# Kernel tuning notes

Measured on AMD Instinct MI355X. Metric: run time of the kernel, lower is better.

The kernel has to match this reference:

```python
import jax, jax.numpy as jnp
import numpy as np

N = 100000   # nodes per type
E = 500000   # edges per edge type
HID = 128    # hidden_channels
H = 4        # heads
D = HID // H # head dim = 32
L = 2        # layers
T = 2        # node types: 0=user, 1=item
R = 2        # edge types: 0=user->item, 1=item->user


def setup_inputs() -> dict:
    key = jax.random.key(0)
    ks = jax.random.split(key, 16)
    s = jnp.float32(0.05)
    f32 = jnp.float32
    return {
        "x_user": jax.random.normal(ks[0], (N, HID), f32),
        "x_item": jax.random.normal(ks[1], (N, HID), f32),
        "W_in": jax.random.normal(ks[2], (T, HID, HID), f32) * s,
        "b_in": jnp.zeros((T, HID), f32),
        "Wk": jax.random.normal(ks[3], (L, T, HID, HID), f32) * s,
        "bk": jnp.zeros((L, T, HID), f32),
        "Wq": jax.random.normal(ks[4], (L, T, HID, HID), f32) * s,
        "bq": jnp.zeros((L, T, HID), f32),
        "Wv": jax.random.normal(ks[5], (L, T, HID, HID), f32) * s,
        "bv": jnp.zeros((L, T, HID), f32),
        "a_rel": jax.random.normal(ks[6], (L, R, H, D, D), f32) * s,
        "m_rel": jax.random.normal(ks[7], (L, R, H, D, D), f32) * s,
        "p_rel": jnp.ones((L, R, H), f32),
        "Wo": jax.random.normal(ks[8], (L, T, HID, HID), f32) * s,
        "bo": jnp.zeros((L, T, HID), f32),
        "skip": jnp.zeros((L, T), f32),
        "edge_ui": jax.random.randint(ks[9], (2, E), 0, N, dtype=jnp.int32),
        "edge_iu": jax.random.randint(ks[10], (2, E), 0, N, dtype=jnp.int32),
    }


def _seg_softmax(logits, seg, n):
    # numerically stable softmax over edges grouped by destination node
    m = jax.ops.segment_max(logits, seg, num_segments=n)            # [N,H]
    m = jnp.where(jnp.isfinite(m), m, jnp.float32(0.0))
    e = jnp.exp(logits - m[seg])                                    # [E,H]
    z = jax.ops.segment_sum(e, seg, num_segments=n)                 # [N,H]
    return e / (z[seg] + jnp.float32(1e-16))


def reference(x_user, x_item, W_in, b_in, Wk, bk, Wq, bq, Wv, bv,
              a_rel, m_rel, p_rel, Wo, bo, skip, edge_ui, edge_iu):
    scale = jnp.float32(1.0 / np.sqrt(D))
    # per-node-type input linear + relu (lin_dict)
    h = [jax.nn.relu(x_user @ W_in[0] + b_in[0]),
         jax.nn.relu(x_item @ W_in[1] + b_in[1])]
    # (edge_type_id, src_type, dst_type, edge_index)
    etypes = [(0, 0, 1, edge_ui), (1, 1, 0, edge_iu)]
    for l in range(L):
        k = [(h[t] @ Wk[l, t] + bk[l, t]).reshape(N, H, D) for t in range(T)]
        q = [(h[t] @ Wq[l, t] + bq[l, t]).reshape(N, H, D) for t in range(T)]
        v = [(h[t] @ Wv[l, t] + bv[l, t]).reshape(N, H, D) for t in range(T)]
        agg = [jnp.zeros((N, H, D), h[0].dtype) for _ in range(T)]
        for r, st, dt, e in etypes:
            src, dst = e[0], e[1]
            # relation-specific transforms applied on node table (N < E)
            k_r = jnp.einsum('nhd,hde->nhe', k[st], a_rel[l, r])
            v_r = jnp.einsum('nhd,hde->nhe', v[st], m_rel[l, r])
            logits = jnp.sum(q[dt][dst] * k_r[src], axis=-1) * p_rel[l, r] * scale  # [E,H]
            alpha = _seg_softmax(logits, dst, N)                                    # [E,H]
            msg = alpha[:, :, None] * v_r[src]                                      # [E,H,D]
            agg[dt] = agg[dt] + jax.ops.segment_sum(msg, dst, num_segments=N)
        h_new = []
        for t in range(T):
            out = agg[t].reshape(N, HID)
            a = jax.nn.gelu(out, approximate=False) @ Wo[l, t] + bo[l, t]
            beta = jax.nn.sigmoid(skip[l, t])
            hn = beta * a + (1.0 - beta) * h[t]
            if l > 0:  # model-level residual (i > 0 in torch code)
                hn = hn + h[t]
            h_new.append(hn)
        h = h_new
    return jnp.stack(h)  # [T, N, HID]
```

## Files before the change

kernel.cpp:

```cpp
#include <hip/hip_runtime.h>
#include <stdint.h>
#include <stdio.h>

#define NN 100000
#define NE 500000
#define HID 128
#define NH 4
#define HD 32
#define LL 2
#define SCANB 1024
#define NB ((NN + SCANB - 1) / SCANB)

typedef unsigned short u16;
typedef unsigned char u8;
typedef unsigned int u32;
typedef __attribute__((ext_vector_type(8))) short bfrag;
typedef __attribute__((ext_vector_type(4))) float f32x4;
typedef __attribute__((ext_vector_type(2))) float f32x2;

__device__ __forceinline__ float b2f(u32 lo16) {
  union { u32 u; float f; } c; c.u = lo16; return c.f;
}
__device__ __forceinline__ u16 f2b(float f) {
  union { float f; u32 u; } c; c.f = f;
  u32 u = c.u;
  u32 r = (u + 0x7FFFu + ((u >> 16) & 1u)) >> 16;
  return (u16)r;
}
__device__ __forceinline__ float geluf(float x) {
  return 0.5f * x * (1.0f + erff(x * 0.70710678118654752f));
}
__device__ __forceinline__ void up8(uint4 a, float* f) {
  f[0] = b2f(a.x << 16); f[1] = b2f(a.x & 0xFFFF0000u);
  f[2] = b2f(a.y << 16); f[3] = b2f(a.y & 0xFFFF0000u);
  f[4] = b2f(a.z << 16); f[5] = b2f(a.z & 0xFFFF0000u);
  f[6] = b2f(a.w << 16); f[7] = b2f(a.w & 0xFFFF0000u);
}

__global__ __launch_bounds__(256) void csr_count(const int* __restrict__ e0,
                                                 const int* __restrict__ e1,
                                                 int* __restrict__ deg) {
  int r = blockIdx.y;
  const int* edges = r ? e1 : e0;
  int e = blockIdx.x * 256 + threadIdx.x;
  if (e < NE) atomicAdd(&deg[(size_t)r * NN + edges[NE + e]], 1);
}

__global__ __launch_bounds__(SCANB) void scan1(const int* __restrict__ deg,
                                               int* __restrict__ rp,
                                               int* __restrict__ bsum) {
  __shared__ int ls[SCANB];
  int r = blockIdx.y;
  int t = threadIdx.x;
  int g = blockIdx.x * SCANB + t;
  int v = (g < NN) ? deg[(size_t)r * NN + g] : 0;
  ls[t] = v;
  __syncthreads();
#pragma unroll
  for (int off = 1; off < SCANB; off <<= 1) {
    int u = (t >= off) ? ls[t - off] : 0;
    __syncthreads();
    ls[t] += u;
    __syncthreads();
  }
  if (g < NN) rp[(size_t)r * (NN + 1) + g] = ls[t] - v;
  if (t == SCANB - 1) bsum[r * NB + blockIdx.x] = ls[t];
}

__global__ __launch_bounds__(128) void scan2(const int* __restrict__ bsum,
                                             int* __restrict__ boff) {
  __shared__ int ls[128];
  int r = blockIdx.y;
  int t = threadIdx.x;
  int v = (t < NB) ? bsum[r * NB + t] : 0;
  ls[t] = v;
  __syncthreads();
#pragma unroll
  for (int off = 1; off < 128; off <<= 1) {
    int u = (t >= off) ? ls[t - off] : 0;
    __syncthreads();
    ls[t] += u;
    __syncthreads();
  }
  if (t < NB) boff[r * NB + t] = ls[t] - v;
}

__global__ __launch_bounds__(SCANB) void scan3(int* __restrict__ rp,
                                               int* __restrict__ cursor,
                                               const int* __restrict__ boff) {
  int r = blockIdx.y;
  int g = blockIdx.x * SCANB + threadIdx.x;
  if (g < NN) {
    int v = rp[(size_t)r * (NN + 1) + g] + boff[r * NB + blockIdx.x];
    rp[(size_t)r * (NN + 1) + g] = v;
    cursor[(size_t)r * NN + g] = v;
  }
  if (g == 0) rp[(size_t)r * (NN + 1) + NN] = NE;
}

__global__ __launch_bounds__(256) void csr_fill(const int* __restrict__ e0,
                                                const int* __restrict__ e1,
                                                int* __restrict__ cursor,
                                                int* __restrict__ s0,
                                                int* __restrict__ s1) {
  int r = blockIdx.y;
  const int* edges = r ? e1 : e0;
  int* srcs = r ? s1 : s0;
  int e = blockIdx.x * 256 + threadIdx.x;
  if (e < NE) {
    int pos = atomicAdd(&cursor[(size_t)r * NN + edges[NE + e]], 1);
    srcs[pos] = edges[e];
  }
}

__global__ __launch_bounds__(256) void hist_deg(const int* __restrict__ rp,
                                                int* __restrict__ hist) {
  __shared__ int lh[64];
  int r = blockIdx.y;
  if (threadIdx.x < 64) lh[threadIdx.x] = 0;
  __syncthreads();
  int d = blockIdx.x * 256 + threadIdx.x;
  if (d < NN) {
    const int* rowptr = rp + (size_t)r * (NN + 1);
    int dg = rowptr[d + 1] - rowptr[d];
    atomicAdd(&lh[dg < 63 ? dg : 63], 1);
  }
  __syncthreads();
  if (threadIdx.x < 64 && lh[threadIdx.x])
    atomicAdd(&hist[r * 64 + threadIdx.x], lh[threadIdx.x]);
}

__global__ __launch_bounds__(64) void scan_hist(const int* __restrict__ hist,
                                                int* __restrict__ hcur) {
  __shared__ int ls[64];
  int r = blockIdx.y;
  int t = threadIdx.x;
  int v = hist[r * 64 + t];
  ls[t] = v;
  __syncthreads();
#pragma unroll
  for (int off = 1; off < 64; off <<= 1) {
    int u = (t >= off) ? ls[t - off] : 0;
    __syncthreads();
    ls[t] += u;
    __syncthreads();
  }
  hcur[r * 64 + t] = ls[t] - v;
}

__global__ __launch_bounds__(256) void scatter_deg(const int* __restrict__ rp,
                                                   int* __restrict__ hcur,
                                                   int* __restrict__ o0,
                                                   int* __restrict__ o1) {
  __shared__ int lh[64];
  __shared__ int lbase[64];
  int r = blockIdx.y;
  int* order = r ? o1 : o0;
  if (threadIdx.x < 64) lh[threadIdx.x] = 0;
  __syncthreads();
  int d = blockIdx.x * 256 + threadIdx.x;
  int dg = 0, rank = 0;
  if (d < NN) {
    const int* rowptr = rp + (size_t)r * (NN + 1);
    dg = rowptr[d + 1] - rowptr[d];
    if (dg > 63) dg = 63;
    rank = atomicAdd(&lh[dg], 1);
  }
  __syncthreads();
  if (threadIdx.x < 64)
    lbase[threadIdx.x] = lh[threadIdx.x] ? atomicAdd(&hcur[r * 64 + threadIdx.x], lh[threadIdx.x]) : 0;
  __syncthreads();
  if (d < NN) order[lbase[dg] + rank] = d;
}

__global__ __launch_bounds__(256) void prep_wT(const float* __restrict__ src, size_t srcStride,
                                               u16* __restrict__ dst, size_t dstStride,
                                               const float* __restrict__ bsrc, int bsStride,
                                               float* __restrict__ bdst, int bdStride,
                                               const float* __restrict__ p_rel_q) {
  int m = blockIdx.y;
  const float* S = src + (size_t)m * srcStride;
  u16* D = dst + (size_t)m * dstStride;
  int idx = blockIdx.x * 256 + threadIdx.x;
  int k = idx >> 7, n = idx & 127;
  float v = S[idx];
  if (p_rel_q != nullptr) {
    int l = m >> 1, t = m & 1;
    v *= p_rel_q[((l << 1) | (1 - t)) * NH + (n >> 5)] * 0.17677669529663687f;
  }
  D[(size_t)n * HID + k] = f2b(v);
  if (bsrc != nullptr && blockIdx.x == 0 && threadIdx.x < HID) {
    int col = threadIdx.x;
    float bvv = bsrc[(size_t)m * bsStride + col];
    if (p_rel_q != nullptr) {
      int l = m >> 1, t = m & 1;
      bvv *= p_rel_q[((l << 1) | (1 - t)) * NH + (col >> 5)] * 0.17677669529663687f;
    }
    bdst[(size_t)m * bdStride + col] = bvv;
  }
}

__global__ __launch_bounds__(256) void combine_all(
    const float* __restrict__ Wk, const float* __restrict__ bk,
    const float* __restrict__ Wv, const float* __restrict__ bv,
    const float* __restrict__ a_rel, const float* __restrict__ m_rel,
    u16* __restrict__ wqkvT, float* __restrict__ bqkv) {
  int l = blockIdx.z;
  int t = blockIdx.y >> 1, which = blockIdx.y & 1;
  const float* W  = (which == 0 ? Wk : Wv) + (size_t)(l * 2 + t) * HID * HID;
  const float* b  = (which == 0 ? bk : bv) + (size_t)(l * 2 + t) * HID;
  const float* Ar = (which == 0 ? a_rel : m_rel) + (size_t)(l * 2 + t) * NH * HD * HD;
  u16* Wd = wqkvT + ((size_t)(l * 2 + t) * 3 + 1 + which) * HID * HID;
  float* bd = bqkv + ((size_t)(l * 2 + t) * 3 + 1 + which) * HID;
  int idx = blockIdx.x * 256 + threadIdx.x;
  int i = idx >> 7, col = idx & 127;
  int h = col >> 5, e = col & 31;
  {
    const float* ap = Ar + h * HD * HD + e;
    const float* wp = W + (size_t)i * HID + h * HD;
    float s = 0.f;
#pragma unroll
    for (int d = 0; d < HD; ++d) s += wp[d] * ap[d * HD];
    Wd[(size_t)col * HID + i] = f2b(s);
  }
  if (blockIdx.x == 0 && threadIdx.x < HID) {
    int col2 = threadIdx.x, h2 = col2 >> 5, e2 = col2 & 31;
    const float* ap = Ar + h2 * HD * HD + e2;
    const float* bp = b + h2 * HD;
    float s = 0.f;
#pragma unroll
    for (int d = 0; d < HD; ++d) s += bp[d] * ap[d * HD];
    bd[col2] = s;
  }
}

__global__ __launch_bounds__(256) void qkv_gemm(
    const u16* __restrict__ h0, const u16* __restrict__ h1,
    const u16* __restrict__ WT,
    const float* __restrict__ bias,
    u16* __restrict__ q0, u16* __restrict__ q1,
    u8* __restrict__ k0, u8* __restrict__ k1,
    u8* __restrict__ v0, u8* __restrict__ v1, int gb) {
  __shared__ __align__(16) u16 sW[2][HID * HID];
  const int t = blockIdx.x >= gb;
  const int bx = t ? blockIdx.x - gb : blockIdx.x;
  const u16* A = t ? h1 : h0;
  const u16* Wg = WT + (size_t)t * 3 * HID * HID;
  const float* bs = bias + (size_t)t * 3 * HID;
  u16* Oq = t ? q1 : q0;
  u8* Ok = t ? k1 : k0;
  u8* Ov = t ? v1 : v0;

  const int lane = threadIdx.x & 63;
  const int wid = threadIdx.x >> 6;
  const int l16 = lane & 15, g = lane >> 4;
  const int rbase = bx * 128 + wid * 32;

  auto stageW = [&](int m, int buf) {
    const u16* Wm = Wg + (size_t)m * HID * HID;
#pragma unroll
    for (int j = 0; j < 8; ++j) {
      int ins = wid * 8 + j;
      int o16 = ins * 64 + lane;
      int row = o16 >> 4, ch = o16 & 15;
      const u16* src = Wm + (size_t)row * HID + ((ch ^ (row & 7)) << 3);
      u16* dst = &sW[buf][0] + (size_t)ins * 512;
      __builtin_amdgcn_global_load_lds(
          (const __attribute__((address_space(1))) unsigned int*)src,
          (__attribute__((address_space(3))) unsigned int*)dst, 16, 0, 0);
    }
  };

  bfrag af[2][4];
  int rowA[2];
#pragma unroll
  for (int rt = 0; rt < 2; ++rt) {
    int row = rbase + rt * 16 + l16;
    rowA[rt] = row;
    int rl = row < NN ? row : NN - 1;
    const bfrag* ap = (const bfrag*)(A + (size_t)rl * HID);
#pragma unroll
    for (int ks = 0; ks < 4; ++ks) af[rt][ks] = ap[ks * 4 + g];
  }

  stageW(0, 0);
  __syncthreads();

#pragma unroll
  for (int m = 0; m < 3; ++m) {
    if (m + 1 < 3) stageW(m + 1, (m + 1) & 1);
    f32x4 acc[2][8];
#pragma unroll
    for (int rt = 0; rt < 2; ++rt)
#pragma unroll
      for (int ct = 0; ct < 8; ++ct) acc[rt][ct] = (f32x4){0.f, 0.f, 0.f, 0.f};
#pragma unroll
    for (int ct = 0; ct < 8; ++ct) {
      int row = ct * 16 + l16;
      bfrag wf[4];
#pragma unroll
      for (int ks = 0; ks < 4; ++ks)
        wf[ks] = *(const bfrag*)&sW[m & 1][(size_t)row * HID +
                                           (((ks * 4 + g) ^ (row & 7)) << 3)];
#pragma unroll
      for (int ks = 0; ks < 4; ++ks)
#pragma unroll
        for (int rt = 0; rt < 2; ++rt)
          acc[rt][ct] = __builtin_amdgcn_mfma_f32_16x16x32_bf16(wf[ks], af[rt][ks],
                                                                acc[rt][ct], 0, 0, 0);
    }
#pragma unroll
    for (int rt = 0; rt < 2; ++rt) {
      int row = rowA[rt];
      if (row >= NN) continue;
#pragma unroll
      for (int ct = 0; ct < 8; ++ct) {
        int nc = ct * 16 + g * 4;
        const float4 bb = *(const float4*)(bs + m * HID + nc);
        float o0 = acc[rt][ct][0] + bb.x;
        float o1 = acc[rt][ct][1] + bb.y;
        float o2 = acc[rt][ct][2] + bb.z;
        float o3 = acc[rt][ct][3] + bb.w;
        if (m == 0) {
          u32 lo = (u32)f2b(o0) | ((u32)f2b(o1) << 16);
          u32 hi = (u32)f2b(o2) | ((u32)f2b(o3) << 16);
          *(uint2*)(Oq + (size_t)row * HID + nc) = make_uint2(lo, hi);
        } else {
          u8* O8 = (m == 1) ? Ok : Ov;
          u32 pk = __builtin_amdgcn_cvt_pk_fp8_f32(o0, o1, 0u, false);
          pk = __builtin_amdgcn_cvt_pk_fp8_f32(o2, o3, pk, true);
          *(u32*)(O8 + (size_t)row * HID + nc) = pk;
        }
      }
    }
    if (m + 1 < 3) __syncthreads();
  }
}

template <int NMAT, bool RELU, bool SKIP, bool FP8KV, bool AF32>
__global__ __launch_bounds__(256) void mfgemm(
    const void* __restrict__ A0, const void* __restrict__ A1, int M, int gb,
    const u16* __restrict__ WT, size_t wtStride,
    const float* __restrict__ bias, size_t biasStride,
    u16* __restrict__ O00, u16* __restrict__ O01, u16* __restrict__ O02,
    u16* __restrict__ O10, u16* __restrict__ O11, u16* __restrict__ O12,
    float* __restrict__ Of0, float* __restrict__ Of1,
    const u16* __restrict__ hp0, const u16* __restrict__ hp1,
    const float* __restrict__ skipP, int resflag) {
  __shared__ __align__(16) u16 sW[HID * HID];
  const int t = blockIdx.x >= gb;
  const int bx = t ? blockIdx.x - gb : blockIdx.x;
  const void* A = t ? A1 : A0;
  const u16* Wg = WT + (size_t)t * wtStride;
  const float* bs = bias + (size_t)t * biasStride;
  u16* Os[3];
  Os[0] = t ? O10 : O00; Os[1] = t ? O11 : O01; Os[2] = t ? O12 : O02;
  float* Of = t ? Of1 : Of0;
  const u16* hprev = t ? hp1 : hp0;

  const int lane = threadIdx.x & 63;
  const int wid = threadIdx.x >> 6;
  const int l16 = lane & 15, g = lane >> 4;
  const int rbase = bx * 128 + wid * 32;

  float beta = 0.f;
  if (SKIP) beta = 1.f / (1.f + __expf(-skipP[t]));

  auto stageW = [&](int m) {
    const u16* Wm = Wg + (size_t)m * HID * HID;
#pragma unroll
    for (int j = 0; j < 8; ++j) {
      int ins = wid * 8 + j;
      int o16 = ins * 64 + lane;
      int row = o16 >> 4, ch = o16 & 15;
      const u16* src = Wm + (size_t)row * HID + ((ch ^ (row & 7)) << 3);
      u16* dst = sW + (size_t)ins * 512;
      __builtin_amdgcn_global_load_lds(
          (const __attribute__((address_space(1))) unsigned int*)src,
          (__attribute__((address_space(3))) unsigned int*)dst, 16, 0, 0);
    }
  };

  bfrag af[2][4];
  int rowA[2];
#pragma unroll
  for (int rt = 0; rt < 2; ++rt) {
    int row = rbase + rt * 16 + l16;
    rowA[rt] = row;
    int rl = row < M ? row : M - 1;
    if (AF32) {
      const float* apf = (const float*)A + (size_t)rl * HID;
#pragma unroll
      for (int ks = 0; ks < 4; ++ks) {
        float4 u0 = *(const float4*)(apf + (ks * 4 + g) * 8);
        float4 u1 = *(const float4*)(apf + (ks * 4 + g) * 8 + 4);
        union { u16 s[8]; bfrag b; } pk;
        pk.s[0] = f2b(u0.x); pk.s[1] = f2b(u0.y); pk.s[2] = f2b(u0.z); pk.s[3] = f2b(u0.w);
        pk.s[4] = f2b(u1.x); pk.s[5] = f2b(u1.y); pk.s[6] = f2b(u1.z); pk.s[7] = f2b(u1.w);
        af[rt][ks] = pk.b;
      }
    } else {
      const bfrag* ap = (const bfrag*)A + (size_t)rl * (HID / 8);
#pragma unroll
      for (int ks = 0; ks < 4; ++ks) af[rt][ks] = ap[ks * 4 + g];
    }
  }

  stageW(0);
  __syncthreads();

#pragma unroll
  for (int m = 0; m < NMAT; ++m) {
    f32x4 acc[2][8];
#pragma unroll
    for (int rt = 0; rt < 2; ++rt)
#pragma unroll
      for (int ct = 0; ct < 8; ++ct) acc[rt][ct] = (f32x4){0.f, 0.f, 0.f, 0.f};
#pragma unroll
    for (int ct = 0; ct < 8; ++ct) {
      int row = ct * 16 + l16;
      bfrag wf[4];
#pragma unroll
      for (int ks = 0; ks < 4; ++ks)
        wf[ks] = *(const bfrag*)&sW[(size_t)row * HID + (((ks * 4 + g) ^ (row & 7)) << 3)];
#pragma unroll
      for (int ks = 0; ks < 4; ++ks)
#pragma unroll
        for (int rt = 0; rt < 2; ++rt)
          acc[rt][ct] = __builtin_amdgcn_mfma_f32_16x16x32_bf16(wf[ks], af[rt][ks],
                                                                acc[rt][ct], 0, 0, 0);
    }
    if (m + 1 < NMAT) {
      __syncthreads();
      stageW(m + 1);
    }
    u16* Ob = Os[m];
#pragma unroll
    for (int rt = 0; rt < 2; ++rt) {
      int row = rowA[rt];
      if (row >= M) continue;
#pragma unroll
      for (int ct = 0; ct < 8; ++ct) {
        int nc = ct * 16 + g * 4;
        const float4 bb = *(const float4*)(bs + m * HID + nc);
        float o0 = acc[rt][ct][0] + bb.x;
        float o1 = acc[rt][ct][1] + bb.y;
        float o2 = acc[rt][ct][2] + bb.z;
        float o3 = acc[rt][ct][3] + bb.w;
        if (RELU) {
          o0 = fmaxf(o0, 0.f); o1 = fmaxf(o1, 0.f);
          o2 = fmaxf(o2, 0.f); o3 = fmaxf(o3, 0.f);
        }
        if (SKIP) {
          uint2 hh2 = *(const uint2*)(hprev + (size_t)row * HID + nc);
          float h0 = b2f(hh2.x << 16), h1 = b2f(hh2.x & 0xFFFF0000u);
          float h2 = b2f(hh2.y << 16), h3 = b2f(hh2.y & 0xFFFF0000u);
          o0 = beta * o0 + (1.f - beta) * h0;
          o1 = beta * o1 + (1.f - beta) * h1;
          o2 = beta * o2 + (1.f - beta) * h2;
          o3 = beta * o3 + (1.f - beta) * h3;
          if (resflag) { o0 += h0; o1 += h1; o2 += h2; o3 += h3; }
        }
        if (FP8KV && m >= 1) {
          u32 pk = __builtin_amdgcn_cvt_pk_fp8_f32(o0, o1, 0u, false);
          pk = __builtin_amdgcn_cvt_pk_fp8_f32(o2, o3, pk, true);
          *(u32*)((u8*)Ob + (size_t)row * HID + nc) = pk;
        } else {
          if (Ob != nullptr) {
            u32 lo = (u32)f2b(o0) | ((u32)f2b(o1) << 16);
            u32 hi = (u32)f2b(o2) | ((u32)f2b(o3) << 16);
            *(uint2*)(Ob + (size_t)row * HID + nc) = make_uint2(lo, hi);
          }
          if (NMAT == 1 && Of != nullptr) {
            *(float4*)(Of + (size_t)row * HID + nc) = make_float4(o0, o1, o2, o3);
          }
        }
      }
    }
    if (m + 1 < NMAT) __syncthreads();
  }
}

__global__ __launch_bounds__(256) void agg_csr(
    const int* __restrict__ rp0, const int* __restrict__ ss0, const int* __restrict__ od0,
    const u16* __restrict__ q0, const u8* __restrict__ k0,
    const u8* __restrict__ v0, u16* __restrict__ o0,
    const int* __restrict__ rp1, const int* __restrict__ ss1, const int* __restrict__ od1,
    const u16* __restrict__ q1, const u8* __restrict__ k1,
    const u8* __restrict__ v1, u16* __restrict__ o1, int agb) {
  const int r = blockIdx.x >= agb;
  const int bx = r ? blockIdx.x - agb : blockIdx.x;
  int i = bx * 256 + threadIdx.x;
  if (i >= NN * NH) return;
  const int* rowptr = r ? rp1 : rp0;
  const int* srcs = r ? ss1 : ss0;
  const int* order = r ? od1 : od0;
  const u16* qT = r ? q1 : q0;
  const u8* kT = r ? k1 : k0;
  const u8* vT = r ? v1 : v0;
  u16* aggb = r ? o1 : o0;

  int dst = order[i >> 2], h = i & 3;
  float qv[HD];
  {
    const uint4* qp = (const uint4*)(qT + (size_t)dst * HID + h * HD);
#pragma unroll
    for (int j = 0; j < 4; ++j) up8(qp[j], qv + j * 8);
  }
  float acc[HD];
#pragma unroll
  for (int j = 0; j < HD; ++j) acc[j] = 0.f;
  float z = 0.f;
  int b = rowptr[dst], e2 = rowptr[dst + 1];
  for (int idx = b; idx < e2; ++idx) {
    int src = srcs[idx];
    const uint4* kp = (const uint4*)(kT + (size_t)src * HID + h * HD);
    const uint4* vp = (const uint4*)(vT + (size_t)src * HID + h * HD);
    uint4 ka0 = kp[0], ka1 = kp[1];
    uint4 va0 = vp[0], va1 = vp[1];
    u32 kw[8] = {ka0.x, ka0.y, ka0.z, ka0.w, ka1.x, ka1.y, ka1.z, ka1.w};
    u32 vw[8] = {va0.x, va0.y, va0.z, va0.w, va1.x, va1.y, va1.z, va1.w};
    float s = 0.f;
#pragma unroll
    for (int j = 0; j < 8; ++j) {
      f32x2 p0 = __builtin_amdgcn_cvt_pk_f32_fp8(kw[j], false);
      f32x2 p1 = __builtin_amdgcn_cvt_pk_f32_fp8(kw[j], true);
      s += qv[4 * j] * p0.x + qv[4 * j + 1] * p0.y + qv[4 * j + 2] * p1.x + qv[4 * j + 3] * p1.y;
    }
    s = fminf(s, 60.f);
    float ev = __expf(s);
    z += ev;
#pragma unroll
    for (int j = 0; j < 8; ++j) {
      f32x2 p0 = __builtin_amdgcn_cvt_pk_f32_fp8(vw[j], false);
      f32x2 p1 = __builtin_amdgcn_cvt_pk_f32_fp8(vw[j], true);
      acc[4 * j] += ev * p0.x; acc[4 * j + 1] += ev * p0.y;
      acc[4 * j + 2] += ev * p1.x; acc[4 * j + 3] += ev * p1.y;
    }
  }
  float inv = 1.f / (z + 1e-16f);
  u16* ap = aggb + (size_t)dst * HID + h * HD;
  u32 w[16];
#pragma unroll
  for (int j = 0; j < 16; ++j) {
    float a0 = geluf(acc[2 * j] * inv);
    float a1 = geluf(acc[2 * j + 1] * inv);
    w[j] = (u32)f2b(a0) | ((u32)f2b(a1) << 16);
  }
#pragma unroll
  for (int j = 0; j < 4; ++j)
    *(uint4*)(ap + j * 8) = make_uint4(w[4 * j], w[4 * j + 1], w[4 * j + 2], w[4 * j + 3]);
}

extern "C" void kernel_launch(void* const* d_in, const int* in_sizes, int n_in,
                              void* d_out, int out_size, void* d_ws, size_t ws_size,
                              hipStream_t stream) {
  const float* x_user = (const float*)d_in[0];
  const float* x_item = (const float*)d_in[1];
  const float* W_in = (const float*)d_in[2];
  const float* b_in = (const float*)d_in[3];
  const float* Wk = (const float*)d_in[4];
  const float* bk = (const float*)d_in[5];
  const float* Wq = (const float*)d_in[6];
  const float* bq = (const float*)d_in[7];
  const float* Wv = (const float*)d_in[8];
  const float* bv = (const float*)d_in[9];
  const float* a_rel = (const float*)d_in[10];
  const float* m_rel = (const float*)d_in[11];
  const float* p_rel = (const float*)d_in[12];
  const float* Wo = (const float*)d_in[13];
  const float* bo = (const float*)d_in[14];
  const float* skipP = (const float*)d_in[15];
  const int* edge_ui = (const int*)d_in[16];
  const int* edge_iu = (const int*)d_in[17];
  float* out = (float*)d_out;

  char* p = (char*)d_ws;
  auto take = [&](size_t bytes) {
    void* r = (void*)p;
    p += (bytes + 255) & ~(size_t)255;
    return r;
  };
  size_t nodeB = (size_t)NN * HID * sizeof(u16);
  size_t node8 = (size_t)NN * HID;
  u16* hb[2] = {(u16*)take(nodeB), (u16*)take(nodeB)};
  u16* qb[2] = {(u16*)take(nodeB), (u16*)take(nodeB)};
  u8* kb[2] = {(u8*)take(node8), (u8*)take(node8)};
  u8* vb[2] = {(u8*)take(node8), (u8*)take(node8)};
  u16* aggb[2] = {(u16*)take(nodeB), (u16*)take(nodeB)};
  int* deg2   = (int*)take((size_t)2 * NN * 4);
  int* cur2   = (int*)take((size_t)2 * NN * 4);
  int* bsum2  = (int*)take((size_t)2 * NB * 4);
  int* boff2  = (int*)take((size_t)2 * NB * 4);
  int* hist2  = (int*)take((size_t)2 * 64 * 4);
  int* hcur2  = (int*)take((size_t)2 * 64 * 4);
  int* rp2    = (int*)take((size_t)2 * (NN + 1) * 4);
  int* srcs[2]  = {(int*)take((size_t)NE * 4), (int*)take((size_t)NE * 4)};
  int* order[2] = {(int*)take((size_t)NN * 4), (int*)take((size_t)NN * 4)};
  u16* winT  = (u16*)take((size_t)2 * HID * HID * 2);
  u16* woT   = (u16*)take((size_t)4 * HID * HID * 2);
  u16* wqkvT = (u16*)take((size_t)2 * 2 * 3 * HID * HID * 2);
  float* bqkv = (float*)take((size_t)2 * 2 * 3 * HID * 4);
  size_t used = (size_t)(p - (char*)d_ws);
  if (used > ws_size) {
    fprintf(stderr, "HGT kernel: workspace too small: need %zu, have %zu\n", used, ws_size);
    return;
  }

  const int GB = (NN + 127) / 128;
  const int EB = (NE + 255) / 256;
  const int DB = (NN + 255) / 256;
  dim3 blk(256);

  hipMemsetAsync(deg2, 0, (size_t)2 * NN * 4, stream);
  csr_count<<<dim3(EB, 2), blk, 0, stream>>>(edge_ui, edge_iu, deg2);
  scan1<<<dim3(NB, 2), SCANB, 0, stream>>>(deg2, rp2, bsum2);
  scan2<<<dim3(1, 2), 128, 0, stream>>>(bsum2, boff2);
  scan3<<<dim3(NB, 2), SCANB, 0, stream>>>(rp2, cur2, boff2);
  csr_fill<<<dim3(EB, 2), blk, 0, stream>>>(edge_ui, edge_iu, cur2, srcs[0], srcs[1]);
  hipMemsetAsync(hist2, 0, 2 * 64 * 4, stream);
  hist_deg<<<dim3(DB, 2), blk, 0, stream>>>(rp2, hist2);
  scan_hist<<<dim3(1, 2), 64, 0, stream>>>(hist2, hcur2);
  scatter_deg<<<dim3(DB, 2), blk, 0, stream>>>(rp2, hcur2, order[0], order[1]);
  int* rowptr[2] = {rp2, rp2 + (NN + 1)};

  prep_wT<<<dim3(64, 2), blk, 0, stream>>>(W_in, HID * HID, winT, HID * HID,
                                           nullptr, 0, nullptr, 0, nullptr);
  prep_wT<<<dim3(64, 4), blk, 0, stream>>>(Wo, HID * HID, woT, HID * HID,
                                           nullptr, 0, nullptr, 0, nullptr);
  prep_wT<<<dim3(64, 4), blk, 0, stream>>>(Wq, HID * HID, wqkvT, 3 * HID * HID,
                                           bq, HID, bqkv, 3 * HID, p_rel);
  combine_all<<<dim3(64, 4, 2), blk, 0, stream>>>(Wk, bk, Wv, bv, a_rel, m_rel,
                                                  wqkvT, bqkv);

  mfgemm<1, true, false, false, true><<<2 * GB, blk, 0, stream>>>(
      x_user, x_item, NN, GB, winT, HID * HID, b_in, HID,
      hb[0], nullptr, nullptr, hb[1], nullptr, nullptr,
      nullptr, nullptr, nullptr, nullptr, nullptr, 0);

  const int AGB = (NN * NH + 255) / 256;
  for (int l = 0; l < LL; ++l) {
    qkv_gemm<<<2 * GB, blk, 0, stream>>>(
        hb[0], hb[1],
        wqkvT + (size_t)l * 2 * 3 * HID * HID,
        bqkv + (size_t)l * 2 * 3 * HID,
        qb[0], qb[1], kb[0], kb[1], vb[0], vb[1], GB);
    agg_csr<<<2 * AGB, blk, 0, stream>>>(
        rowptr[0], srcs[0], order[0], qb[1], kb[0], vb[0], aggb[1],
        rowptr[1], srcs[1], order[1], qb[0], kb[1], vb[1], aggb[0], AGB);
    if (l == 0) {
      mfgemm<1, false, true, false, false><<<2 * GB, blk, 0, stream>>>(
          aggb[0], aggb[1], NN, GB,
          woT, HID * HID, bo, HID,
          hb[0], nullptr, nullptr, hb[1], nullptr, nullptr,
          nullptr, nullptr, hb[0], hb[1], skipP, 0);
    } else {
      mfgemm<1, false, true, false, false><<<2 * GB, blk, 0, stream>>>(
          aggb[0], aggb[1], NN, GB,
          woT + (size_t)2 * HID * HID, HID * HID, bo + 2 * HID, HID,
          nullptr, nullptr, nullptr, nullptr, nullptr, nullptr,
          out, out + (size_t)NN * HID, hb[0], hb[1], skipP + 2, 1);
    }
  }
}
```

Before: 528.1 us.

## Fuse preprocessing kernels and unroll edge loop by two in aggregation

Folds the degree histogram, its scan and the degree-bucket scatter into the existing CSR scan kernels, and merges the four weight-prep launches into a single prep_all kernel. This cuts kernel launches and one memset from the setup phase. The aggregation loop now handles two edges per iteration, issuing loads for both before computing, to expose more memory-level parallelism in the gather. In exchange, the unrolled loop uses more registers.

```diff
diff --git a/kernel.cpp b/kernel.cpp
--- a/kernel.cpp
+++ b/kernel.cpp
@@ -36,10 +36,33 @@
   f[4] = b2f(a.z << 16); f[5] = b2f(a.z & 0xFFFF0000u);
   f[6] = b2f(a.w << 16); f[7] = b2f(a.w & 0xFFFF0000u);
 }
+__device__ __forceinline__ float dot32(uint4 a, uint4 b, const float* qv) {
+  u32 w[8] = {a.x, a.y, a.z, a.w, b.x, b.y, b.z, b.w};
+  float s = 0.f;
+#pragma unroll
+  for (int j = 0; j < 8; ++j) {
+    f32x2 p0 = __builtin_amdgcn_cvt_pk_f32_fp8(w[j], false);
+    f32x2 p1 = __builtin_amdgcn_cvt_pk_f32_fp8(w[j], true);
+    s += qv[4 * j] * p0.x + qv[4 * j + 1] * p0.y + qv[4 * j + 2] * p1.x + qv[4 * j + 3] * p1.y;
+  }
+  return s;
+}
+__device__ __forceinline__ void acc32(uint4 a, uint4 b, float ev, float* acc) {
+  u32 w[8] = {a.x, a.y, a.z, a.w, b.x, b.y, b.z, b.w};
+#pragma unroll
+  for (int j = 0; j < 8; ++j) {
+    f32x2 p0 = __builtin_amdgcn_cvt_pk_f32_fp8(w[j], false);
+    f32x2 p1 = __builtin_amdgcn_cvt_pk_f32_fp8(w[j], true);
+    acc[4 * j] += ev * p0.x; acc[4 * j + 1] += ev * p0.y;
+    acc[4 * j + 2] += ev * p1.x; acc[4 * j + 3] += ev * p1.y;
+  }
+}
 
 __global__ __launch_bounds__(256) void csr_count(const int* __restrict__ e0,
                                                  const int* __restrict__ e1,
-                                                 int* __restrict__ deg) {
+                                                 int* __restrict__ deg,
+                                                 int* __restrict__ hist) {
+  if (blockIdx.x == 0 && blockIdx.y == 0 && threadIdx.x < 128) hist[threadIdx.x] = 0;
   int r = blockIdx.y;
   const int* edges = r ? e1 : e0;
   int e = blockIdx.x * 256 + threadIdx.x;
@@ -48,14 +71,18 @@
 
 __global__ __launch_bounds__(SCANB) void scan1(const int* __restrict__ deg,
                                                int* __restrict__ rp,
-                                               int* __restrict__ bsum) {
+                                               int* __restrict__ bsum,
+                                               int* __restrict__ hist) {
   __shared__ int ls[SCANB];
+  __shared__ int lh[64];
   int r = blockIdx.y;
   int t = threadIdx.x;
   int g = blockIdx.x * SCANB + t;
   int v = (g < NN) ? deg[(size_t)r * NN + g] : 0;
   ls[t] = v;
-  __syncthreads();
+  if (t < 64) lh[t] = 0;
+  __syncthreads();
+  if (g < NN) atomicAdd(&lh[v < 63 ? v : 63], 1);
 #pragma unroll
   for (int off = 1; off < SCANB; off <<= 1) {
     int u = (t >= off) ? ls[t - off] : 0;
@@ -65,10 +92,13 @@
   }
   if (g < NN) rp[(size_t)r * (NN + 1) + g] = ls[t] - v;
   if (t == SCANB - 1) bsum[r * NB + blockIdx.x] = ls[t];
+  if (t < 64 && lh[t]) atomicAdd(&hist[r * 64 + t], lh[t]);
 }
 
 __global__ __launch_bounds__(128) void scan2(const int* __restrict__ bsum,
-                                             int* __restrict__ boff) {
+                                             int* __restrict__ boff,
+                                             const int* __restrict__ hist,
+                                             int* __restrict__ hcur) {
   __shared__ int ls[128];
   int r = blockIdx.y;
   int t = threadIdx.x;
@@ -83,19 +113,51 @@
     __syncthreads();
   }
   if (t < NB) boff[r * NB + t] = ls[t] - v;
+  __syncthreads();
+  int hv = (t < 64) ? hist[r * 64 + t] : 0;
+  ls[t] = hv;
+  __syncthreads();
+#pragma unroll
+  for (int off = 1; off < 64; off <<= 1) {
+    int u = (t >= off) ? ls[t - off] : 0;
+    __syncthreads();
+    ls[t] += u;
+    __syncthreads();
+  }
+  if (t < 64) hcur[r * 64 + t] = ls[t] - hv;
 }
 
 __global__ __launch_bounds__(SCANB) void scan3(int* __restrict__ rp,
                                                int* __restrict__ cursor,
-                                               const int* __restrict__ boff) {
+                                               const int* __restrict__ boff,
+                                               const int* __restrict__ deg,
+                                               int* __restrict__ hcur,
+                                               int* __restrict__ o0,
+                                               int* __restrict__ o1) {
+  __shared__ int lh[64];
+  __shared__ int lbase[64];
   int r = blockIdx.y;
-  int g = blockIdx.x * SCANB + threadIdx.x;
+  int* order = r ? o1 : o0;
+  int t = threadIdx.x;
+  int g = blockIdx.x * SCANB + t;
+  if (t < 64) lh[t] = 0;
+  int dg = 0;
   if (g < NN) {
     int v = rp[(size_t)r * (NN + 1) + g] + boff[r * NB + blockIdx.x];
     rp[(size_t)r * (NN + 1) + g] = v;
     cursor[(size_t)r * NN + g] = v;
+    dg = deg[(size_t)r * NN + g];
+    if (dg > 63) dg = 63;
   }
   if (g == 0) rp[(size_t)r * (NN + 1) + NN] = NE;
+  __syncthreads();
+  int rank = 0;
+  if (g < NN) rank = atomicAdd(&lh[dg], 1);
+  __syncthreads();
+  if (t < 64)
+    lbase[t] = lh[t] ? atomicAdd(&hcur[r * 64 + t], lh[t]) : 0;
+  __syncthreads();
+  if (g < NN) order[lbase[dg] + rank] = g;
 }
 
 __global__ __launch_bounds__(256) void csr_fill(const int* __restrict__ e0,
@@ -113,124 +175,71 @@
   }
 }
 
-__global__ __launch_bounds__(256) void hist_deg(const int* __restrict__ rp,
-                                                int* __restrict__ hist) {
-  __shared__ int lh[64];
-  int r = blockIdx.y;
-  if (threadIdx.x < 64) lh[threadIdx.x] = 0;
-  __syncthreads();
-  int d = blockIdx.x * 256 + threadIdx.x;
-  if (d < NN) {
-    const int* rowptr = rp + (size_t)r * (NN + 1);
-    int dg = rowptr[d + 1] - rowptr[d];
-    atomicAdd(&lh[dg < 63 ? dg : 63], 1);
-  }
-  __syncthreads();
-  if (threadIdx.x < 64 && lh[threadIdx.x])
-    atomicAdd(&hist[r * 64 + threadIdx.x], lh[threadIdx.x]);
-}
-
-__global__ __launch_bounds__(64) void scan_hist(const int* __restrict__ hist,
-                                                int* __restrict__ hcur) {
-  __shared__ int ls[64];
-  int r = blockIdx.y;
-  int t = threadIdx.x;
-  int v = hist[r * 64 + t];
-  ls[t] = v;
-  __syncthreads();
-#pragma unroll
-  for (int off = 1; off < 64; off <<= 1) {
-    int u = (t >= off) ? ls[t - off] : 0;
-    __syncthreads();
-    ls[t] += u;
-    __syncthreads();
-  }
-  hcur[r * 64 + t] = ls[t] - v;
-}
-
-__global__ __launch_bounds__(256) void scatter_deg(const int* __restrict__ rp,
-                                                   int* __restrict__ hcur,
-                                                   int* __restrict__ o0,
-                                                   int* __restrict__ o1) {
-  __shared__ int lh[64];
-  __shared__ int lbase[64];
-  int r = blockIdx.y;
-  int* order = r ? o1 : o0;
-  if (threadIdx.x < 64) lh[threadIdx.x] = 0;
-  __syncthreads();
-  int d = blockIdx.x * 256 + threadIdx.x;
-  int dg = 0, rank = 0;
-  if (d < NN) {
-    const int* rowptr = rp + (size_t)r * (NN + 1);
-    dg = rowptr[d + 1] - rowptr[d];
-    if (dg > 63) dg = 63;
-    rank = atomicAdd(&lh[dg], 1);
-  }
-  __syncthreads();
-  if (threadIdx.x < 64)
-    lbase[threadIdx.x] = lh[threadIdx.x] ? atomicAdd(&hcur[r * 64 + threadIdx.x], lh[threadIdx.x]) : 0;
-  __syncthreads();
-  if (d < NN) order[lbase[dg] + rank] = d;
-}
-
-__global__ __launch_bounds__(256) void prep_wT(const float* __restrict__ src, size_t srcStride,
-                                               u16* __restrict__ dst, size_t dstStride,
-                                               const float* __restrict__ bsrc, int bsStride,
-                                               float* __restrict__ bdst, int bdStride,
-                                               const float* __restrict__ p_rel_q) {
-  int m = blockIdx.y;
-  const float* S = src + (size_t)m * srcStride;
-  u16* D = dst + (size_t)m * dstStride;
-  int idx = blockIdx.x * 256 + threadIdx.x;
-  int k = idx >> 7, n = idx & 127;
-  float v = S[idx];
-  if (p_rel_q != nullptr) {
-    int l = m >> 1, t = m & 1;
-    v *= p_rel_q[((l << 1) | (1 - t)) * NH + (n >> 5)] * 0.17677669529663687f;
-  }
-  D[(size_t)n * HID + k] = f2b(v);
-  if (bsrc != nullptr && blockIdx.x == 0 && threadIdx.x < HID) {
-    int col = threadIdx.x;
-    float bvv = bsrc[(size_t)m * bsStride + col];
-    if (p_rel_q != nullptr) {
-      int l = m >> 1, t = m & 1;
-      bvv *= p_rel_q[((l << 1) | (1 - t)) * NH + (col >> 5)] * 0.17677669529663687f;
-    }
-    bdst[(size_t)m * bdStride + col] = bvv;
-  }
-}
-
-__global__ __launch_bounds__(256) void combine_all(
+__global__ __launch_bounds__(256) void prep_all(
+    const float* __restrict__ W_in,
+    const float* __restrict__ Wo,
+    const float* __restrict__ Wq, const float* __restrict__ bq,
     const float* __restrict__ Wk, const float* __restrict__ bk,
     const float* __restrict__ Wv, const float* __restrict__ bv,
     const float* __restrict__ a_rel, const float* __restrict__ m_rel,
+    const float* __restrict__ p_rel,
+    u16* __restrict__ winT, u16* __restrict__ woT,
     u16* __restrict__ wqkvT, float* __restrict__ bqkv) {
-  int l = blockIdx.z;
-  int t = blockIdx.y >> 1, which = blockIdx.y & 1;
-  const float* W  = (which == 0 ? Wk : Wv) + (size_t)(l * 2 + t) * HID * HID;
-  const float* b  = (which == 0 ? bk : bv) + (size_t)(l * 2 + t) * HID;
-  const float* Ar = (which == 0 ? a_rel : m_rel) + (size_t)(l * 2 + t) * NH * HD * HD;
-  u16* Wd = wqkvT + ((size_t)(l * 2 + t) * 3 + 1 + which) * HID * HID;
-  float* bd = bqkv + ((size_t)(l * 2 + t) * 3 + 1 + which) * HID;
+  const float scale = 0.17677669529663687f;
+  int y = blockIdx.y;
   int idx = blockIdx.x * 256 + threadIdx.x;
-  int i = idx >> 7, col = idx & 127;
-  int h = col >> 5, e = col & 31;
-  {
-    const float* ap = Ar + h * HD * HD + e;
-    const float* wp = W + (size_t)i * HID + h * HD;
-    float s = 0.f;
-#pragma unroll
-    for (int d = 0; d < HD; ++d) s += wp[d] * ap[d * HD];
-    Wd[(size_t)col * HID + i] = f2b(s);
-  }
-  if (blockIdx.x == 0 && threadIdx.x < HID) {
-    int col2 = threadIdx.x, h2 = col2 >> 5, e2 = col2 & 31;
-    const float* ap = Ar + h2 * HD * HD + e2;
-    const float* bp = b + h2 * HD;
-    float s = 0.f;
-#pragma unroll
-    for (int d = 0; d < HD; ++d) s += bp[d] * ap[d * HD];
-    bd[col2] = s;
+  if (y < 10) {
+    const float* src; u16* dst;
+    const float* bsrc = nullptr; float* bdst = nullptr;
+    bool useP = false; int m = 0;
+    if (y < 2) {
+      m = y; src = W_in + (size_t)m * HID * HID; dst = winT + (size_t)m * HID * HID;
+    } else if (y < 6) {
+      m = y - 2; src = Wo + (size_t)m * HID * HID; dst = woT + (size_t)m * HID * HID;
+    } else {
+      m = y - 6; src = Wq + (size_t)m * HID * HID;
+      dst = wqkvT + (size_t)m * 3 * HID * HID;
+      useP = true; bsrc = bq + (size_t)m * HID; bdst = bqkv + (size_t)m * 3 * HID;
+    }
+    int k = idx >> 7, n = idx & 127;
+    float v = src[idx];
+    if (useP) {
+      int l = m >> 1, t = m & 1;
+      v *= p_rel[((l << 1) | (1 - t)) * NH + (n >> 5)] * scale;
+    }
+    dst[(size_t)n * HID + k] = f2b(v);
+    if (bdst != nullptr && blockIdx.x == 0 && threadIdx.x < HID) {
+      int col = threadIdx.x;
+      int l = m >> 1, t = m & 1;
+      bdst[col] = bsrc[col] * p_rel[((l << 1) | (1 - t)) * NH + (col >> 5)] * scale;
+    }
+  } else {
+    int c = y - 10;
+    int l = c >> 2, t = (c >> 1) & 1, which = c & 1;
+    const float* W  = (which == 0 ? Wk : Wv) + (size_t)(l * 2 + t) * HID * HID;
+    const float* b  = (which == 0 ? bk : bv) + (size_t)(l * 2 + t) * HID;
+    const float* Ar = (which == 0 ? a_rel : m_rel) + (size_t)(l * 2 + t) * NH * HD * HD;
+    u16* Wd = wqkvT + ((size_t)(l * 2 + t) * 3 + 1 + which) * HID * HID;
+    float* bd = bqkv + ((size_t)(l * 2 + t) * 3 + 1 + which) * HID;
+    int i = idx >> 7, col = idx & 127;
+    int h = col >> 5, e = col & 31;
+    {
+      const float* ap = Ar + h * HD * HD + e;
+      const float* wp = W + (size_t)i * HID + h * HD;
+      float s = 0.f;
+#pragma unroll
+      for (int d = 0; d < HD; ++d) s += wp[d] * ap[d * HD];
+      Wd[(size_t)col * HID + i] = f2b(s);
+    }
+    if (blockIdx.x == 0 && threadIdx.x < HID) {
+      int col2 = threadIdx.x, h2 = col2 >> 5, e2 = col2 & 31;
+      const float* ap = Ar + h2 * HD * HD + e2;
+      const float* bp = b + h2 * HD;
+      float s = 0.f;
+#pragma unroll
+      for (int d = 0; d < HD; ++d) s += bp[d] * ap[d * HD];
+      bd[col2] = s;
+    }
   }
 }
 
@@ -512,31 +521,35 @@
   for (int j = 0; j < HD; ++j) acc[j] = 0.f;
   float z = 0.f;
   int b = rowptr[dst], e2 = rowptr[dst + 1];
-  for (int idx = b; idx < e2; ++idx) {
-    int src = srcs[idx];
-    const uint4* kp = (const uint4*)(kT + (size_t)src * HID + h * HD);
-    const uint4* vp = (const uint4*)(vT + (size_t)src * HID + h * HD);
-    uint4 ka0 = kp[0], ka1 = kp[1];
-    uint4 va0 = vp[0], va1 = vp[1];
-    u32 kw[8] = {ka0.x, ka0.y, ka0.z, ka0.w, ka1.x, ka1.y, ka1.z, ka1.w};
-    u32 vw[8] = {va0.x, va0.y, va0.z, va0.w, va1.x, va1.y, va1.z, va1.w};
-    float s = 0.f;
-#pragma unroll
-    for (int j = 0; j < 8; ++j) {
-      f32x2 p0 = __builtin_amdgcn_cvt_pk_f32_fp8(kw[j], false);
-      f32x2 p1 = __builtin_amdgcn_cvt_pk_f32_fp8(kw[j], true);
-      s += qv[4 * j] * p0.x + qv[4 * j + 1] * p0.y + qv[4 * j + 2] * p1.x + qv[4 * j + 3] * p1.y;
-    }
-    s = fminf(s, 60.f);
-    float ev = __expf(s);
-    z += ev;
-#pragma unroll
-    for (int j = 0; j < 8; ++j) {
-      f32x2 p0 = __builtin_amdgcn_cvt_pk_f32_fp8(vw[j], false);
-      f32x2 p1 = __builtin_amdgcn_cvt_pk_f32_fp8(vw[j], true);
-      acc[4 * j] += ev * p0.x; acc[4 * j + 1] += ev * p0.y;
-      acc[4 * j + 2] += ev * p1.x; acc[4 * j + 3] += ev * p1.y;
-    }
+  int idx = b;
+  for (; idx + 2 <= e2; idx += 2) {
+    int s0 = srcs[idx], s1 = srcs[idx + 1];
+    const uint4* kp0 = (const uint4*)(kT + (size_t)s0 * HID + h * HD);
+    const uint4* vp0 = (const uint4*)(vT + (size_t)s0 * HID + h * HD);
+    const uint4* kp1 = (const uint4*)(kT + (size_t)s1 * HID + h * HD);
+    const uint4* vp1 = (const uint4*)(vT + (size_t)s1 * HID + h * HD);
+    uint4 kA = kp0[0], kB = kp0[1];
+    uint4 kC = kp1[0], kD = kp1[1];
+    uint4 vA = vp0[0], vB = vp0[1];
+    uint4 vC = vp1[0], vD = vp1[1];
+    float d0 = dot32(kA, kB, qv);
+    float d1 = dot32(kC, kD, qv);
+    float ev0 = __expf(fminf(d0, 60.f));
+    float ev1 = __expf(fminf(d1, 60.f));
+    z += ev0 + ev1;
+    acc32(vA, vB, ev0, acc);
+    acc32(vC, vD, ev1, acc);
+  }
+  if (idx < e2) {
+    int s0 = srcs[idx];
+    const uint4* kp0 = (const uint4*)(kT + (size_t)s0 * HID + h * HD);
+    const uint4* vp0 = (const uint4*)(vT + (size_t)s0 * HID + h * HD);
+    uint4 kA = kp0[0], kB = kp0[1];
+    uint4 vA = vp0[0], vB = vp0[1];
+    float d0 = dot32(kA, kB, qv);
+    float ev0 = __expf(fminf(d0, 60.f));
+    z += ev0;
+    acc32(vA, vB, ev0, acc);
   }
   float inv = 1.f / (z + 1e-16f);
   u16* ap = aggb + (size_t)dst * HID + h * HD;
@@ -609,29 +622,19 @@
 
   const int GB = (NN + 127) / 128;
   const int EB = (NE + 255) / 256;
-  const int DB = (NN + 255) / 256;
   dim3 blk(256);
 
   hipMemsetAsync(deg2, 0, (size_t)2 * NN * 4, stream);
-  csr_count<<<dim3(EB, 2), blk, 0, stream>>>(edge_ui, edge_iu, deg2);
-  scan1<<<dim3(NB, 2), SCANB, 0, stream>>>(deg2, rp2, bsum2);
-  scan2<<<dim3(1, 2), 128, 0, stream>>>(bsum2, boff2);
-  scan3<<<dim3(NB, 2), SCANB, 0, stream>>>(rp2, cur2, boff2);
+  prep_all<<<dim3(64, 18), blk, 0, stream>>>(W_in, Wo, Wq, bq, Wk, bk, Wv, bv,
+                                             a_rel, m_rel, p_rel,
+                                             winT, woT, wqkvT, bqkv);
+  csr_count<<<dim3(EB, 2), blk, 0, stream>>>(edge_ui, edge_iu, deg2, hist2);
+  scan1<<<dim3(NB, 2), SCANB, 0, stream>>>(deg2, rp2, bsum2, hist2);
+  scan2<<<dim3(1, 2), 128, 0, stream>>>(bsum2, boff2, hist2, hcur2);
+  scan3<<<dim3(NB, 2), SCANB, 0, stream>>>(rp2, cur2, boff2, deg2, hcur2,
+                                           order[0], order[1]);
   csr_fill<<<dim3(EB, 2), blk, 0, stream>>>(edge_ui, edge_iu, cur2, srcs[0], srcs[1]);
-  hipMemsetAsync(hist2, 0, 2 * 64 * 4, stream);
-  hist_deg<<<dim3(DB, 2), blk, 0, stream>>>(rp2, hist2);
-  scan_hist<<<dim3(1, 2), 64, 0, stream>>>(hist2, hcur2);
-  scatter_deg<<<dim3(DB, 2), blk, 0, stream>>>(rp2, hcur2, order[0], order[1]);
   int* rowptr[2] = {rp2, rp2 + (NN + 1)};
-
-  prep_wT<<<dim3(64, 2), blk, 0, stream>>>(W_in, HID * HID, winT, HID * HID,
-                                           nullptr, 0, nullptr, 0, nullptr);
-  prep_wT<<<dim3(64, 4), blk, 0, stream>>>(Wo, HID * HID, woT, HID * HID,
-                                           nullptr, 0, nullptr, 0, nullptr);
-  prep_wT<<<dim3(64, 4), blk, 0, stream>>>(Wq, HID * HID, wqkvT, 3 * HID * HID,
-                                           bq, HID, bqkv, 3 * HID, p_rel);
-  combine_all<<<dim3(64, 4, 2), blk, 0, stream>>>(Wk, bk, Wv, bv, a_rel, m_rel,
-                                                  wqkvT, bqkv);
 
   mfgemm<1, true, false, false, true><<<2 * GB, blk, 0, stream>>>(
       x_user, x_item, NN, GB, winT, HID * HID, b_in, HID,
```

After: 509.4 us. 1.04x faster.
